# Optimization experiments

Measured on AMD Instinct MI355X. Metric: run time of the kernel, lower is better.

Reference implementation:

```python
import jax, jax.numpy as jnp
import numpy as np

B, D, TC, TE, TGT = 8, 256, 2048, 2048, 256
SCALE = 16.0  # sqrt(256.0) hardcoded in the original module


def setup_inputs() -> dict:
    key = jax.random.key(0)
    k1, k2, k3 = jax.random.split(key, 3)
    content_emb = jax.random.normal(k1, (B, D, TC), dtype=jnp.float32)
    emotion_emb = jax.random.normal(k2, (B, D, TE), dtype=jnp.float32)
    # Conv1d(embed_dim*2 -> target_embed, kernel=3): weight [out, in, k]
    fan_in = 2 * D * 3
    conv_w = jax.random.normal(k3, (TGT, 2 * D, 3), dtype=jnp.float32) / np.sqrt(fan_in)
    conv_b = jnp.zeros((TGT,), dtype=jnp.float32)
    return {"content_emb": content_emb, "emotion_emb": emotion_emb,
            "conv_w": conv_w, "conv_b": conv_b}


def reference(content_emb, emotion_emb, conv_w, conv_b):
    # (B, D, T) -> (B, T, D)
    c = jnp.transpose(content_emb, (0, 2, 1))   # [B, Tc, D]
    e = jnp.transpose(emotion_emb, (0, 2, 1))   # [B, Te, D]
    sim = jnp.einsum('btd,bsd->bts', c, e)      # [B, Tc, Te]
    attn = jax.nn.softmax(sim / SCALE, axis=-1)
    weighted_emo = jnp.einsum('bts,bsd->btd', attn, e)  # [B, Tc, D]
    x = jnp.concatenate([c, weighted_emo], axis=-1)     # [B, Tc, 2D]
    x = jnp.transpose(x, (0, 2, 1))                     # [B, 2D, Tc]
    out = jax.lax.conv_general_dilated(
        x, conv_w, window_strides=(1,), padding=[(1, 1)],
        dimension_numbers=('NCH', 'OIH', 'NCH'))
    return out + conv_b[None, :, None]
```

## Files before the change

kernel.cpp:

```cpp
#include <hip/hip_runtime.h>

typedef __bf16 bf16x8 __attribute__((ext_vector_type(8)));
typedef __bf16 bf16x4 __attribute__((ext_vector_type(4)));
typedef float  f32x4  __attribute__((ext_vector_type(4)));

#define MFMA(a, b, c) __builtin_amdgcn_mfma_f32_16x16x32_bf16((a), (b), (c), 0, 0, 0)
#define DRAIN_VMCNT()  __builtin_amdgcn_s_waitcnt(0x0F70)
#define WAIT_VMCNT_2() __builtin_amdgcn_s_waitcnt(0x0F72)

constexpr int Bc  = 8;
constexpr int D   = 256;
constexpr int TC  = 2048;
constexpr int TE  = 2048;
constexpr int TGT = 256;
constexpr int XR  = 256;

#define EXP_C 0.09016844005556021f

__device__ __forceinline__ void gl_lds16(const __bf16* g, __bf16* l) {
  __builtin_amdgcn_global_load_lds(
      (const __attribute__((address_space(1))) void*)g,
      (__attribute__((address_space(3))) void*)l, 16, 0, 0);
}

__global__ void k_prep_all(const float* __restrict__ content,
                           const float* __restrict__ emotion,
                           __bf16* __restrict__ xcat,
                           __bf16* __restrict__ e_t, __bf16* __restrict__ e_ds2,
                           const float* __restrict__ w, __bf16* __restrict__ Wk) {
  __shared__ __bf16 tile[64][68];
  const int tid = threadIdx.x;

  if (blockIdx.y == TC / 64) {
    const int base = (blockIdx.z * 8 + blockIdx.x) * 2048;
#pragma unroll
    for (int j = 0; j < 8; ++j) {
      const int idx = base + j * 256 + tid;
      const int o = idx >> 9, i = idx & 511;
#pragma unroll
      for (int k = 0; k < 3; ++k)
        Wk[k * (TGT * 512) + idx] = (__bf16)w[(size_t)o * 1536 + i * 3 + k];
    }
    return;
  }

  const int b   = blockIdx.x;
  const int t0  = blockIdx.y * 64;
  const int sec = blockIdx.z;
  const bool isC = sec < 4;
  const int d0 = (sec & 3) * 64;
  const int c4 = (tid & 15) * 4;
  const int r0 = tid >> 4;
  const float* sp = (isC ? content : emotion) + ((size_t)b * D + d0) * 2048 + t0;
#pragma unroll
  for (int i = 0; i < 4; ++i) {
    const int r = r0 + 16 * i;
    const float4 v = *(const float4*)(sp + (size_t)r * 2048 + c4);
    bf16x4 pv;
    pv[0] = (__bf16)v.x; pv[1] = (__bf16)v.y; pv[2] = (__bf16)v.z; pv[3] = (__bf16)v.w;
    *(bf16x4*)&tile[r][c4] = pv;
  }
  __syncthreads();

  __bf16* dp = (isC ? xcat + ((size_t)b * TC + t0) * XR
                    : e_t + ((size_t)b * TE + t0) * D) + d0;
#pragma unroll
  for (int i = 0; i < 2; ++i) {
    const int idx = tid + 256 * i;
    const int r   = idx >> 3;
    const int c8  = (idx & 7) * 8;
    bf16x8 v;
#pragma unroll
    for (int j = 0; j < 8; ++j) v[j] = tile[c8 + j][r];
    *(bf16x8*)(dp + (size_t)r * 256 + c8) = v;
  }

  if (!isC) {
    const int row = tid >> 2, sc = tid & 3;
#pragma unroll
    for (int h = 0; h < 2; ++h) {
      bf16x4 lo = *(const bf16x4*)&tile[row][h * 32 + sc * 8];
      bf16x4 hi = *(const bf16x4*)&tile[row][h * 32 + sc * 8 + 4];
      bf16x8 v;
      v[0] = lo[0]; v[1] = lo[1]; v[2] = lo[2]; v[3] = lo[3];
      v[4] = hi[0]; v[5] = hi[1]; v[6] = hi[2]; v[7] = hi[3];
      __bf16* qp = e_ds2 +
          ((((size_t)b * 64 + (t0 >> 5) + h) * 256 + d0 + row) << 5) + sc * 8;
      *(bf16x8*)qp = v;
    }
  }
}

__global__ __launch_bounds__(256, 2) void k_attn(const __bf16* __restrict__ xcat,
                                                 const __bf16* __restrict__ e_t,
                                                 const __bf16* __restrict__ e_ds2,
                                                 __bf16* __restrict__ Op,
                                                 float* __restrict__ Lp) {
  __shared__ __align__(16) __bf16 sEt[2][8192];
  __shared__ __align__(16) __bf16 sEs[2][8192];
  __shared__ __align__(16) __bf16 sP[4][2][640];

  const int tid  = threadIdx.x;
  const int lane = tid & 63;
  const int w    = tid >> 6;
  const int q    = lane >> 4;
  const int tl   = lane & 15;
  const int b    = blockIdx.x & 7;
  const int xt   = (blockIdx.x >> 3) | (blockIdx.y << 1);
  const int z    = blockIdx.z;
  const int tbase = xt * 128 + w * 32;

  const __bf16* etb  = e_t  + (size_t)b * TE * D;
  const __bf16* esb2 = e_ds2 + (size_t)b * 64 * 8192;

  bf16x8 cB[2][8];
#pragma unroll
  for (int tt = 0; tt < 2; ++tt) {
    const __bf16* crow = xcat + ((size_t)(b * TC) + tbase + tt * 16 + tl) * XR + q * 8;
#pragma unroll
    for (int ks = 0; ks < 8; ++ks) cB[tt][ks] = *(const bf16x8*)(crow + ks * 32);
  }

  unsigned offEt[4], offEs[4];
#pragma unroll
  for (int c = 0; c < 4; ++c) {
    const int id = (w * 4 + c) * 64 + lane;
    const int ss = id >> 5, cs = id & 31;
    offEt[c] = ss * D + (cs ^ (ss & 7)) * 8;
    const int dd = id >> 2, ps = id & 3;
    offEs[c] = dd * 32 + (ps ^ ((dd >> 2) & 3)) * 8;
  }

  f32x4 accO[2][16];
#pragma unroll
  for (int tt = 0; tt < 2; ++tt)
#pragma unroll
    for (int dt = 0; dt < 16; ++dt) accO[tt][dt] = (f32x4){0.f, 0.f, 0.f, 0.f};
  float lacc[2] = {0.f, 0.f};

  const int sbase = z * (TE / 4);
  const int sw3 = (tl >> 2) & 3;

  auto stage = [&](int buf, int s0) {
    const __bf16* et = etb + (size_t)s0 * D;
    const __bf16* es = esb2 + ((size_t)(s0 >> 5)) * 8192;
#pragma unroll
    for (int c = 0; c < 4; ++c) {
      gl_lds16(et + offEt[c], &sEt[buf][(w * 4 + c) * 512]);
      gl_lds16(es + offEs[c], &sEs[buf][(w * 4 + c) * 512]);
    }
  };

  stage(0, sbase);
  DRAIN_VMCNT();
  __syncthreads();

  int cur = 0;
  for (int k = 0; k < TE / 128; ++k) {
    if (k < TE / 128 - 1) stage(cur ^ 1, sbase + (k + 1) * 32);

    f32x4 aS[2][2];
#pragma unroll
    for (int i = 0; i < 2; ++i)
#pragma unroll
      for (int j = 0; j < 2; ++j) aS[i][j] = (f32x4){0.f, 0.f, 0.f, 0.f};
    const __bf16* pe = &sEt[cur][0];
#pragma unroll
    for (int ks = 0; ks < 8; ++ks) {
      const int ch = (ks * 4 + q) ^ (tl & 7);
      bf16x8 a0 = *(const bf16x8*)(pe + (tl * 32 + ch) * 8);
      bf16x8 a1 = *(const bf16x8*)(pe + ((16 + tl) * 32 + ch) * 8);
      aS[0][0] = MFMA(a0, cB[0][ks], aS[0][0]);
      aS[0][1] = MFMA(a0, cB[1][ks], aS[0][1]);
      aS[1][0] = MFMA(a1, cB[0][ks], aS[1][0]);
      aS[1][1] = MFMA(a1, cB[1][ks], aS[1][1]);
    }

#pragma unroll
    for (int tt = 0; tt < 2; ++tt) {
      bf16x4 w0, w1;
#pragma unroll
      for (int r = 0; r < 4; ++r) {
        float e0 = exp2f(aS[0][tt][r] * EXP_C);
        float e1 = exp2f(aS[1][tt][r] * EXP_C);
        lacc[tt] += e0 + e1;
        w0[r] = (__bf16)e0;
        w1[r] = (__bf16)e1;
      }
      __bf16* pw = &sP[w][tt][tl * 40 + q * 4];
      *(bf16x4*)pw = w0;
      *(bf16x4*)(pw + 16) = w1;
    }
    bf16x8 pB0 = *(const bf16x8*)(&sP[w][0][tl * 40 + q * 8]);
    bf16x8 pB1 = *(const bf16x8*)(&sP[w][1][tl * 40 + q * 8]);

    const __bf16* ps = &sEs[cur][0];
#pragma unroll
    for (int dt = 0; dt < 16; ++dt) {
      bf16x8 a = *(const bf16x8*)(ps + ((dt * 16 + tl) * 4 + (q ^ sw3)) * 8);
      accO[0][dt] = MFMA(a, pB0, accO[0][dt]);
      accO[1][dt] = MFMA(a, pB1, accO[1][dt]);
    }

    DRAIN_VMCNT();
    __syncthreads();
    cur ^= 1;
  }

#pragma unroll
  for (int tt = 0; tt < 2; ++tt) {
    float v = lacc[tt];
    v += __shfl_xor(v, 16, 64);
    v += __shfl_xor(v, 32, 64);
    const size_t rowl = (size_t)b * TC + tbase + tt * 16 + tl;
    if (q == 0) Lp[rowl * 4 + z] = v;
    __bf16* orow = Op + (rowl * 4 + z) * D + q * 4;
#pragma unroll
    for (int dt = 0; dt < 16; ++dt) {
      bf16x4 o;
#pragma unroll
      for (int r = 0; r < 4; ++r) o[r] = (__bf16)accO[tt][dt][r];
      *(bf16x4*)(orow + dt * 16) = o;
    }
  }
}

__global__ __launch_bounds__(512, 2) void k_conv(const __bf16* __restrict__ xcat,
                                                 const __bf16* __restrict__ Op,
                                                 const float* __restrict__ Lp,
                                                 const __bf16* __restrict__ Wk,
                                                 const float* __restrict__ bias,
                                                 float* __restrict__ out) {
  __shared__ __align__(16) __bf16 sXA[66 * 256];
  __shared__ __align__(16) __bf16 sXB[66 * 256];
  __shared__ __align__(16) __bf16 sW[3][8192];
  const int tid  = threadIdx.x;
  const int lane = tid & 63;
  const int wv   = tid >> 6;
  const int wo   = wv & 3;
  const int wt   = wv >> 2;
  const int q    = lane >> 4;
  const int tl   = lane & 15;
  const int b    = blockIdx.x & 7;
  const int t0   = (blockIdx.x >> 3) * 64;
  const int o0   = wo * 64;
  const int sw3  = (tl >> 2) & 3;
  const int rh   = lane >> 5;
  const int l5   = lane & 31;

  const __bf16* xb = xcat + (size_t)b * TC * XR;
  for (int i = wv; i < 33; i += 8) {
    const int rl = 2 * i + rh;
    int gr = t0 - 1 + rl;
    gr = gr < 0 ? 0 : (gr > TC - 1 ? TC - 1 : gr);
    const int cs = l5 ^ (rl & 7);
    gl_lds16(xb + (size_t)gr * XR + cs * 8, &sXA[i * 512]);
  }

  unsigned offW[2];
#pragma unroll
  for (int c = 0; c < 2; ++c) {
    const int id = (wv * 2 + c) * 64 + lane;
    const int o = id >> 2, ps = id & 3;
    offW[c] = o * 512 + (ps ^ ((o >> 2) & 3)) * 8;
  }
  auto stageW = [&](int buf, int s) {
    const int kk = s >> 4, is = s & 15;
    const __bf16* wb = Wk + (size_t)kk * TGT * 512 + is * 32;
#pragma unroll
    for (int c = 0; c < 2; ++c)
      gl_lds16(wb + offW[c], &sW[buf][(wv * 2 + c) * 512]);
  };
  stageW(0, 0);
  stageW(1, 1);

  for (int i = wv; i < 33; i += 8) {
    const int rl = 2 * i + rh;
    int gr = t0 - 1 + rl;
    gr = gr < 0 ? 0 : (gr > TC - 1 ? TC - 1 : gr);
    const size_t row = (size_t)b * TC + gr;
    const float4 lv = *(const float4*)(Lp + row * 4);
    const float inv = 1.0f / (lv.x + lv.y + lv.z + lv.w);
    float a8[8] = {0.f, 0.f, 0.f, 0.f, 0.f, 0.f, 0.f, 0.f};
#pragma unroll
    for (int zz = 0; zz < 4; ++zz) {
      bf16x8 a = *(const bf16x8*)(Op + (row * 4 + zz) * D + l5 * 8);
#pragma unroll
      for (int r = 0; r < 8; ++r) a8[r] += (float)a[r];
    }
    bf16x8 o;
#pragma unroll
    for (int r = 0; r < 8; ++r) o[r] = (__bf16)(a8[r] * inv);
    *(bf16x8*)((char*)&sXB[rl * 256] + ((l5 * 16) ^ ((rl & 7) << 4))) = o;
  }

  DRAIN_VMCNT();
  __syncthreads();

  if (t0 == 0 && tid < 256) { sXA[tid] = (__bf16)0.f; sXB[tid] = (__bf16)0.f; }
  if (t0 + 64 == TC && tid < 256) {
    sXA[65 * 256 + tid] = (__bf16)0.f; sXB[65 * 256 + tid] = (__bf16)0.f;
  }
  __syncthreads();

  f32x4 acc[4][2];
#pragma unroll
  for (int mt = 0; mt < 4; ++mt) {
#pragma unroll
    for (int r = 0; r < 4; ++r) {
      const float bv = bias[o0 + mt * 16 + q * 4 + r];
#pragma unroll
      for (int nt = 0; nt < 2; ++nt) acc[mt][nt][r] = bv;
    }
  }

  int cur = 0;
  for (int s = 0; s < 48; ++s) {
    if (s < 46) stageW((cur + 2) % 3, s + 2);
    const int kk = s >> 4, is = s & 15;
    const __bf16* pl = (is & 8) ? sXB : sXA;
    const int cbyte = (is & 7) * 64 + q * 16;
    bf16x8 bfr[2];
#pragma unroll
    for (int nt = 0; nt < 2; ++nt) {
      const int t = wt * 32 + nt * 16 + tl + kk;
      bfr[nt] = *(const bf16x8*)((const char*)pl + t * 512 + (cbyte ^ ((t & 7) << 4)));
    }
#pragma unroll
    for (int mt = 0; mt < 4; ++mt) {
      const int o = o0 + mt * 16 + tl;
      bf16x8 af = *(const bf16x8*)(&sW[cur][(o * 4 + (q ^ sw3)) * 8]);
#pragma unroll
      for (int nt = 0; nt < 2; ++nt) acc[mt][nt] = MFMA(af, bfr[nt], acc[mt][nt]);
    }
    if (s < 46) WAIT_VMCNT_2(); else DRAIN_VMCNT();
    __builtin_amdgcn_s_barrier();
    __builtin_amdgcn_sched_barrier(0);
    cur = cur == 2 ? 0 : cur + 1;
  }

#pragma unroll
  for (int mt = 0; mt < 4; ++mt) {
#pragma unroll
    for (int nt = 0; nt < 2; ++nt) {
#pragma unroll
      for (int r = 0; r < 4; ++r) {
        const int o = o0 + mt * 16 + q * 4 + r;
        const int t = t0 + wt * 32 + nt * 16 + tl;
        out[((size_t)b * TGT + o) * TC + t] = acc[mt][nt][r];
      }
    }
  }
}

extern "C" void kernel_launch(void* const* d_in, const int* in_sizes, int n_in,
                              void* d_out, int out_size, void* d_ws, size_t ws_size,
                              hipStream_t stream) {
  (void)in_sizes; (void)n_in; (void)out_size; (void)ws_size;
  const float* content = (const float*)d_in[0];
  const float* emotion = (const float*)d_in[1];
  const float* conv_w  = (const float*)d_in[2];
  const float* conv_b  = (const float*)d_in[3];
  float* out = (float*)d_out;

  char* ws = (char*)d_ws;
  __bf16* xcat = (__bf16*)ws;
  __bf16* Wk   = (__bf16*)(ws + 8388608);
  __bf16* Op   = (__bf16*)(ws + 9437184);
  float*  Lp   = (float*)(ws + 42991616);
  __bf16* e_t   = (__bf16*)d_out;
  __bf16* e_ds2 = (__bf16*)((char*)d_out + 8388608);

  k_prep_all<<<dim3(Bc, TC / 64 + 1, 8), 256, 0, stream>>>(
      content, emotion, xcat, e_t, e_ds2, conv_w, Wk);
  k_attn<<<dim3(TC / 128, Bc, 4), 256, 0, stream>>>(xcat, e_t, e_ds2, Op, Lp);
  k_conv<<<dim3((TC / 64) * Bc), 512, 0, stream>>>(xcat, Op, Lp, Wk, conv_b, out);
}
```

Baseline: 171.9 us.

## Stage one emotion tile and read transposed operand via ds_read_b64_tr_b16 with triple buffering

The emotion data was previously written twice, once row-major and once as a transposed copy, and each step loaded both copies into LDS. Now a single tiled layout is written, and the PV matmul operand is produced with the LDS transpose-read instruction, which halves global and LDS staging traffic. The staging pipeline also goes from double to triple buffering with partial vmcnt waits. This adds custom asm, manual lgkmcnt waits and a more intricate layout whose correctness depends on exact index maths.

```diff
diff --git a/kernel.cpp b/kernel.cpp
--- a/kernel.cpp
+++ b/kernel.cpp
@@ -5,8 +5,10 @@
 typedef float  f32x4  __attribute__((ext_vector_type(4)));
 
 #define MFMA(a, b, c) __builtin_amdgcn_mfma_f32_16x16x32_bf16((a), (b), (c), 0, 0, 0)
+#define WAIT_VMCNT(n)  __builtin_amdgcn_s_waitcnt(0x0F70 | (n))
 #define DRAIN_VMCNT()  __builtin_amdgcn_s_waitcnt(0x0F70)
 #define WAIT_VMCNT_2() __builtin_amdgcn_s_waitcnt(0x0F72)
+#define BARRIER() do { __builtin_amdgcn_s_barrier(); __builtin_amdgcn_sched_barrier(0); } while (0)
 
 constexpr int Bc  = 8;
 constexpr int D   = 256;
@@ -23,10 +25,15 @@
       (__attribute__((address_space(3))) void*)l, 16, 0, 0);
 }
 
+__device__ __forceinline__ bf16x4 tr_b64(unsigned addr) {
+  bf16x4 d;
+  asm volatile("ds_read_b64_tr_b16 %0, %1" : "=v"(d) : "v"(addr));
+  return d;
+}
+
 __global__ void k_prep_all(const float* __restrict__ content,
                            const float* __restrict__ emotion,
-                           __bf16* __restrict__ xcat,
-                           __bf16* __restrict__ e_t, __bf16* __restrict__ e_ds2,
+                           __bf16* __restrict__ xcat, __bf16* __restrict__ e_t2,
                            const float* __restrict__ w, __bf16* __restrict__ Wk) {
   __shared__ __bf16 tile[64][68];
   const int tid = threadIdx.x;
@@ -62,42 +69,42 @@
   }
   __syncthreads();
 
-  __bf16* dp = (isC ? xcat + ((size_t)b * TC + t0) * XR
-                    : e_t + ((size_t)b * TE + t0) * D) + d0;
-#pragma unroll
-  for (int i = 0; i < 2; ++i) {
-    const int idx = tid + 256 * i;
-    const int r   = idx >> 3;
-    const int c8  = (idx & 7) * 8;
-    bf16x8 v;
-#pragma unroll
-    for (int j = 0; j < 8; ++j) v[j] = tile[c8 + j][r];
-    *(bf16x8*)(dp + (size_t)r * 256 + c8) = v;
-  }
-
-  if (!isC) {
-    const int row = tid >> 2, sc = tid & 3;
-#pragma unroll
-    for (int h = 0; h < 2; ++h) {
-      bf16x4 lo = *(const bf16x4*)&tile[row][h * 32 + sc * 8];
-      bf16x4 hi = *(const bf16x4*)&tile[row][h * 32 + sc * 8 + 4];
+  if (isC) {
+    __bf16* dp = xcat + ((size_t)b * TC + t0) * XR + d0;
+#pragma unroll
+    for (int i = 0; i < 2; ++i) {
+      const int idx = tid + 256 * i;
+      const int r   = idx >> 3;
+      const int c8  = (idx & 7) * 8;
       bf16x8 v;
-      v[0] = lo[0]; v[1] = lo[1]; v[2] = lo[2]; v[3] = lo[3];
-      v[4] = hi[0]; v[5] = hi[1]; v[6] = hi[2]; v[7] = hi[3];
-      __bf16* qp = e_ds2 +
-          ((((size_t)b * 64 + (t0 >> 5) + h) * 256 + d0 + row) << 5) + sc * 8;
+#pragma unroll
+      for (int j = 0; j < 8; ++j) v[j] = tile[c8 + j][r];
+      *(bf16x8*)(dp + (size_t)r * 256 + c8) = v;
+    }
+  } else {
+    __bf16* base = e_t2 + (size_t)b * TE * D + (size_t)(t0 >> 5) * 8192
+                   + (size_t)(d0 >> 4) * 256;
+#pragma unroll
+    for (int i = 0; i < 2; ++i) {
+      const int idx = tid + 256 * i;
+      const int r   = idx >> 3;
+      const int dc  = idx & 7;
+      bf16x8 v;
+#pragma unroll
+      for (int j = 0; j < 8; ++j) v[j] = tile[dc * 8 + j][r];
+      __bf16* qp = base + (r >> 5) * 8192
+                   + ((((r >> 4) & 1) * 16 + (dc >> 1)) * 16 + (r & 15)) * 16
+                   + (dc & 1) * 8;
       *(bf16x8*)qp = v;
     }
   }
 }
 
 __global__ __launch_bounds__(256, 2) void k_attn(const __bf16* __restrict__ xcat,
-                                                 const __bf16* __restrict__ e_t,
-                                                 const __bf16* __restrict__ e_ds2,
+                                                 const __bf16* __restrict__ e_t2,
                                                  __bf16* __restrict__ Op,
                                                  float* __restrict__ Lp) {
-  __shared__ __align__(16) __bf16 sEt[2][8192];
-  __shared__ __align__(16) __bf16 sEs[2][8192];
+  __shared__ __align__(16) __bf16 sT[3][8192];
   __shared__ __align__(16) __bf16 sP[4][2][640];
 
   const int tid  = threadIdx.x;
@@ -110,8 +117,7 @@
   const int z    = blockIdx.z;
   const int tbase = xt * 128 + w * 32;
 
-  const __bf16* etb  = e_t  + (size_t)b * TE * D;
-  const __bf16* esb2 = e_ds2 + (size_t)b * 64 * 8192;
+  const __bf16* etb = e_t2 + (size_t)b * TE * D;
 
   bf16x8 cB[2][8];
 #pragma unroll
@@ -121,15 +127,9 @@
     for (int ks = 0; ks < 8; ++ks) cB[tt][ks] = *(const bf16x8*)(crow + ks * 32);
   }
 
-  unsigned offEt[4], offEs[4];
-#pragma unroll
-  for (int c = 0; c < 4; ++c) {
-    const int id = (w * 4 + c) * 64 + lane;
-    const int ss = id >> 5, cs = id & 31;
-    offEt[c] = ss * D + (cs ^ (ss & 7)) * 8;
-    const int dd = id >> 2, ps = id & 3;
-    offEs[c] = dd * 32 + (ps ^ ((dd >> 2) & 3)) * 8;
-  }
+  unsigned offT[4];
+#pragma unroll
+  for (int c = 0; c < 4; ++c) offT[c] = ((w * 4 + c) * 64 + lane) * 8;
 
   f32x4 accO[2][16];
 #pragma unroll
@@ -139,37 +139,40 @@
   float lacc[2] = {0.f, 0.f};
 
   const int sbase = z * (TE / 4);
-  const int sw3 = (tl >> 2) & 3;
 
   auto stage = [&](int buf, int s0) {
-    const __bf16* et = etb + (size_t)s0 * D;
-    const __bf16* es = esb2 + ((size_t)(s0 >> 5)) * 8192;
-#pragma unroll
-    for (int c = 0; c < 4; ++c) {
-      gl_lds16(et + offEt[c], &sEt[buf][(w * 4 + c) * 512]);
-      gl_lds16(es + offEs[c], &sEs[buf][(w * 4 + c) * 512]);
-    }
+    const __bf16* src = etb + (size_t)(s0 >> 5) * 8192;
+#pragma unroll
+    for (int c = 0; c < 4; ++c)
+      gl_lds16(src + offT[c], &sT[buf][(w * 4 + c) * 512]);
   };
 
   stage(0, sbase);
-  DRAIN_VMCNT();
-  __syncthreads();
+  stage(1, sbase + 32);
+  WAIT_VMCNT(4);
+  BARRIER();
+
+  const int p1off = (q >> 1) * 256 + tl * 16 + (q & 1) * 8;
+  const unsigned troff = 128u * (unsigned)q + 8u * (unsigned)tl;
 
   int cur = 0;
-  for (int k = 0; k < TE / 128; ++k) {
-    if (k < TE / 128 - 1) stage(cur ^ 1, sbase + (k + 1) * 32);
+  for (int k = 0; k < 16; ++k) {
+    if (k < 14) {
+      int nb = cur + 2; if (nb >= 3) nb -= 3;
+      stage(nb, sbase + (k + 2) * 32);
+    }
+    const __bf16* pe = &sT[cur][0];
 
     f32x4 aS[2][2];
 #pragma unroll
     for (int i = 0; i < 2; ++i)
 #pragma unroll
       for (int j = 0; j < 2; ++j) aS[i][j] = (f32x4){0.f, 0.f, 0.f, 0.f};
-    const __bf16* pe = &sEt[cur][0];
 #pragma unroll
     for (int ks = 0; ks < 8; ++ks) {
-      const int ch = (ks * 4 + q) ^ (tl & 7);
-      bf16x8 a0 = *(const bf16x8*)(pe + (tl * 32 + ch) * 8);
-      bf16x8 a1 = *(const bf16x8*)(pe + ((16 + tl) * 32 + ch) * 8);
+      const __bf16* pa = pe + ks * 512 + p1off;
+      bf16x8 a0 = *(const bf16x8*)pa;
+      bf16x8 a1 = *(const bf16x8*)(pa + 4096);
       aS[0][0] = MFMA(a0, cB[0][ks], aS[0][0]);
       aS[0][1] = MFMA(a0, cB[1][ks], aS[0][1]);
       aS[1][0] = MFMA(a1, cB[0][ks], aS[1][0]);
@@ -191,20 +194,44 @@
       *(bf16x4*)pw = w0;
       *(bf16x4*)(pw + 16) = w1;
     }
-    bf16x8 pB0 = *(const bf16x8*)(&sP[w][0][tl * 40 + q * 8]);
-    bf16x8 pB1 = *(const bf16x8*)(&sP[w][1][tl * 40 + q * 8]);
-
-    const __bf16* ps = &sEs[cur][0];
-#pragma unroll
-    for (int dt = 0; dt < 16; ++dt) {
-      bf16x8 a = *(const bf16x8*)(ps + ((dt * 16 + tl) * 4 + (q ^ sw3)) * 8);
-      accO[0][dt] = MFMA(a, pB0, accO[0][dt]);
-      accO[1][dt] = MFMA(a, pB1, accO[1][dt]);
-    }
-
-    DRAIN_VMCNT();
-    __syncthreads();
-    cur ^= 1;
+    bf16x4 lo0 = *(const bf16x4*)(&sP[w][0][tl * 40 + q * 4]);
+    bf16x4 hi0 = *(const bf16x4*)(&sP[w][0][tl * 40 + 16 + q * 4]);
+    bf16x4 lo1 = *(const bf16x4*)(&sP[w][1][tl * 40 + q * 4]);
+    bf16x4 hi1 = *(const bf16x4*)(&sP[w][1][tl * 40 + 16 + q * 4]);
+    bf16x8 pB0, pB1;
+#pragma unroll
+    for (int r = 0; r < 4; ++r) {
+      pB0[r] = lo0[r]; pB0[4 + r] = hi0[r];
+      pB1[r] = lo1[r]; pB1[4 + r] = hi1[r];
+    }
+
+    const unsigned abase = (unsigned)(uintptr_t)pe + troff;
+#pragma unroll
+    for (int g = 0; g < 4; ++g) {
+      bf16x4 t0[4], t1[4];
+#pragma unroll
+      for (int d4 = 0; d4 < 4; ++d4) {
+        const unsigned o = abase + (unsigned)((g * 4 + d4) * 512);
+        t0[d4] = tr_b64(o);
+        t1[d4] = tr_b64(o + 8192u);
+      }
+      asm volatile("s_waitcnt lgkmcnt(0)" ::: "memory");
+      __builtin_amdgcn_sched_barrier(0);
+#pragma unroll
+      for (int d4 = 0; d4 < 4; ++d4) {
+        const int dt = g * 4 + d4;
+        bf16x8 af;
+#pragma unroll
+        for (int r = 0; r < 4; ++r) { af[r] = t0[d4][r]; af[4 + r] = t1[d4][r]; }
+        accO[0][dt] = MFMA(af, pB0, accO[0][dt]);
+        accO[1][dt] = MFMA(af, pB1, accO[1][dt]);
+      }
+    }
+
+    if (k < 14)      WAIT_VMCNT(4);
+    else if (k == 14) WAIT_VMCNT(0);
+    if (k < 15) BARRIER();
+    cur += 1; if (cur == 3) cur = 0;
   }
 
 #pragma unroll
@@ -368,11 +395,10 @@
   __bf16* Wk   = (__bf16*)(ws + 8388608);
   __bf16* Op   = (__bf16*)(ws + 9437184);
   float*  Lp   = (float*)(ws + 42991616);
-  __bf16* e_t   = (__bf16*)d_out;
-  __bf16* e_ds2 = (__bf16*)((char*)d_out + 8388608);
+  __bf16* e_t2 = (__bf16*)d_out;
 
   k_prep_all<<<dim3(Bc, TC / 64 + 1, 8), 256, 0, stream>>>(
-      content, emotion, xcat, e_t, e_ds2, conv_w, Wk);
-  k_attn<<<dim3(TC / 128, Bc, 4), 256, 0, stream>>>(xcat, e_t, e_ds2, Op, Lp);
+      content, emotion, xcat, e_t2, conv_w, Wk);
+  k_attn<<<dim3(TC / 128, Bc, 4), 256, 0, stream>>>(xcat, e_t2, Op, Lp);
   k_conv<<<dim3((TC / 64) * Bc), 512, 0, stream>>>(xcat, Op, Lp, Wk, conv_b, out);
 }
```

Measured after the change: 167.2 us. -2.7%, faster.
